# Optimization experiments

Measured on AMD Instinct MI355X. Metric: run time of the kernel, lower is better.

Reference implementation:

```python
import jax, jax.numpy as jnp
import numpy as np
from jax import lax

FILTERS = 8

def _conv(x, k):
    # x: (B,H,W,Cin), k: (KH,KW,Cin,Cout), SAME padding, stride 1
    return lax.conv_general_dilated(x, k, (1, 1), 'SAME',
                                    dimension_numbers=('NHWC', 'HWIO', 'NHWC'))

def _hard_sigmoid(x):
    # keras hard_sigmoid: clip(0.2*x + 0.5, 0, 1)
    return jnp.clip(0.2 * x + 0.5, 0.0, 1.0)


def setup_inputs() -> dict:
    key = jax.random.key(0)
    ks = jax.random.split(key, 4)
    B, T, H, W, C = 32, 16, 64, 64, 3
    x = jax.random.normal(ks[0], (B, T, H, W, C), dtype=jnp.float32)
    W_x = jax.random.normal(ks[1], (3, 3, C, 4 * FILTERS), dtype=jnp.float32) * 0.1
    W_h = jax.random.normal(ks[2], (3, 3, FILTERS, 4 * FILTERS), dtype=jnp.float32) * 0.1
    b = jnp.zeros((4 * FILTERS,), dtype=jnp.float32)
    W_out = jax.random.normal(ks[3], (H * W * FILTERS, 4), dtype=jnp.float32) * 0.02
    b_out = jnp.zeros((4,), dtype=jnp.float32)
    return {"x": x, "W_x": W_x, "W_h": W_h, "b": b, "W_out": W_out, "b_out": b_out}


def reference(x, W_x, W_h, b, W_out, b_out):
    B, T, H, W, C = x.shape
    F = FILTERS

    def step(carry, xt):
        h, c = carry
        z = _conv(xt, W_x) + _conv(h, W_h) + b  # (B,H,W,4F)
        zi, zf, zc, zo = jnp.split(z, 4, axis=-1)  # keras gate order: i, f, c, o
        i = _hard_sigmoid(zi)
        f = _hard_sigmoid(zf)
        c = f * c + i * jnp.tanh(zc)
        o = _hard_sigmoid(zo)
        h = o * jnp.tanh(c)
        return (h, c), None

    h0 = jnp.zeros((B, H, W, F), dtype=x.dtype)
    c0 = jnp.zeros((B, H, W, F), dtype=x.dtype)
    xs = jnp.moveaxis(x, 1, 0)  # (T,B,H,W,C)
    (h_final, _), _ = lax.scan(step, (h0, c0), xs)

    flat = h_final.reshape(B, -1)  # (B, H*W*F)
    logits = flat @ W_out + b_out
    return jax.nn.softmax(logits, axis=-1)
```

## Files before the change

### kernel.cpp

```cpp
#include <hip/hip_runtime.h>
#include <math.h>

#define NB 32
#define NT 16

typedef _Float16 f16;
typedef _Float16 half2f __attribute__((ext_vector_type(2)));
typedef _Float16 half4f __attribute__((ext_vector_type(4)));
typedef _Float16 half8f __attribute__((ext_vector_type(8)));
typedef float    floatx2 __attribute__((ext_vector_type(2)));
typedef float    floatx4 __attribute__((ext_vector_type(4)));

#define XPAD_OFF  0u
#define HPAD0_OFF 18382848u
#define HPAD1_OFF 20680704u
#define CBUF_OFF  22978560u
#define WBQ_OFF   27172864u
#define PART_OFF  27181056u
#define WS_NEED   27197440u

#define BAND0   0
#define BAND1   10880
#define CLDS_OFF 21760
#define REDF_OFF 38144
#define SMEM4    38272

__device__ __forceinline__ float hard_sigmoid(float v) {
    return fminf(fmaxf(fmaf(0.2f, v, 0.5f), 0.0f), 1.0f);
}
__device__ __forceinline__ float fast_tanh(float v) {
    float e = __builtin_amdgcn_exp2f(v * 2.8853900817779268f);
    return 1.0f - 2.0f * __builtin_amdgcn_rcpf(e + 1.0f);
}

__device__ __forceinline__ float wb_entry(int i, const float* Wx,
                                          const float* Wh, const float* bias) {
    int e = i & 7, l = (i >> 3) & 63, n = (i >> 9) & 1, j = i >> 10;
    int h = l >> 4;
    int rr = l & 15;
    int g = (rr & 3) * 8 + 2 * (rr >> 2) + n;
    float wv = 0.f;
    if (j == 0) {
        wv = Wh[(h * 8 + e) * 32 + g];
    } else if (j == 1) {
        wv = Wh[((4 + h) * 8 + e) * 32 + g];
    } else if (j == 2 && h == 0) {
        wv = Wh[(64 + e) * 32 + g];
    } else if (j == 3 && h == 3) {
        wv = (e == 3) ? bias[g] : 0.f;
    } else {
        int ty, txp;
        if (j == 2) { ty = (h == 3) ? 1 : 0; txp = (h == 2) ? 2 : 0; }
        else        { ty = (h == 0) ? 1 : 2; txp = (h == 1) ? 0 : 2; }
        int txq = txp + (e >> 2), c = e & 3;
        if (txq < 3 && c < 3)
            wv = Wx[((ty * 3 + txq) * 3 + c) * 32 + g];
    }
    return wv;
}

#define LDX(base, off) ({                                                  \
    half4f lo_ = *(const half4f*)((base) + (off));                         \
    half4f hi_ = *(const half4f*)((base) + (off) + 8);                     \
    __builtin_shufflevector(lo_, hi_, 0, 1, 2, 3, 4, 5, 6, 7); })

#define GATE_BODY(A0, A1, A2, A3, COLD0, COLD1, CC0, CC1, HH0, HH1)        \
    {                                                                      \
        floatx4 acc0 = {0.f, 0.f, 0.f, 0.f};                               \
        floatx4 acc1 = {0.f, 0.f, 0.f, 0.f};                               \
        acc0 = __builtin_amdgcn_mfma_f32_16x16x32_f16(B00, A0, acc0,0,0,0);\
        acc1 = __builtin_amdgcn_mfma_f32_16x16x32_f16(B01, A0, acc1,0,0,0);\
        acc0 = __builtin_amdgcn_mfma_f32_16x16x32_f16(B10, A1, acc0,0,0,0);\
        acc1 = __builtin_amdgcn_mfma_f32_16x16x32_f16(B11, A1, acc1,0,0,0);\
        acc0 = __builtin_amdgcn_mfma_f32_16x16x32_f16(B20, A2, acc0,0,0,0);\
        acc1 = __builtin_amdgcn_mfma_f32_16x16x32_f16(B21, A2, acc1,0,0,0);\
        acc0 = __builtin_amdgcn_mfma_f32_16x16x32_f16(B30, A3, acc0,0,0,0);\
        acc1 = __builtin_amdgcn_mfma_f32_16x16x32_f16(B31, A3, acc1,0,0,0);\
        float ig0 = hard_sigmoid(acc0[0]), fg0 = hard_sigmoid(acc0[1]);    \
        float cg0 = fast_tanh(acc0[2]),    og0 = hard_sigmoid(acc0[3]);    \
        CC0 = fmaf(fg0, COLD0, ig0 * cg0);                                 \
        HH0 = og0 * fast_tanh(CC0);                                        \
        float ig1 = hard_sigmoid(acc1[0]), fg1 = hard_sigmoid(acc1[1]);    \
        float cg1 = fast_tanh(acc1[2]),    og1 = hard_sigmoid(acc1[3]);    \
        CC1 = fmaf(fg1, COLD1, ig1 * cg1);                                 \
        HH1 = og1 * fast_tanh(CC1);                                        \
    }

__global__ __launch_bounds__(256) void init_all(
    const float* __restrict__ x,
    const float* __restrict__ Wx, const float* __restrict__ Wh,
    const float* __restrict__ bias,
    f16* __restrict__ xpad, f16* __restrict__ h0, f16* __restrict__ h1,
    f16* __restrict__ WB)
{
    int i = blockIdx.x * 256 + threadIdx.x;
    if (i < 200704) {
        int bt = i / 392, p = i - bt * 392;
        int rr, cc;
        if (p < 136) { rr = (p < 68) ? 0 : 65; cc = p - ((p < 68) ? 0 : 68); }
        else { int q = p - 136; rr = 1 + (q >> 2); int m = q & 3;
               cc = (m == 0) ? 0 : 64 + m; }
        half4f v = {0, 0, 0, (f16)1.0f};
        *(half4f*)(xpad + ((size_t)(bt * 66 + rr) * 68 + cc) * 4) = v;
    } else if (i < 225792) {
        int k = i - 200704;
        int buf = k / 12544; k -= buf * 12544;
        int b = k / 392, p = k - b * 392;
        int rr, cc;
        if (p < 136) { rr = (p < 68) ? 0 : 65; cc = p - ((p < 68) ? 0 : 68); }
        else { int q = p - 136; rr = 1 + (q >> 2); int m = q & 3;
               cc = (m == 0) ? 0 : 64 + m; }
        f16* hp = buf ? h1 : h0;
        half8f zz = {0, 0, 0, 0, 0, 0, 0, 0};
        *(half8f*)(hp + ((size_t)(b * 66 + rr) * 68 + cc) * 8) = zz;
    } else if (i < 229888) {
        int k = i - 225792;
        WB[k] = (f16)wb_entry(k, Wx, Wh, bias);
    } else if (i < 754176) {
        int j = i - 229888;
        int b = j >> 14;
        int rem = j & 16383;
        int s = rem >> 12, px = rem & 4095;
        const float* xp = x + ((size_t)(b * 16 + s) * 4096 + px) * 3;
        half4f v = {(f16)xp[0], (f16)xp[1], (f16)xp[2], (f16)1.0f};
        int gr = px >> 6, gc = px & 63;
        *(half4f*)(xpad + ((size_t)((b * 16 + s) * 66 + gr + 1) * 68 + gc + 1) * 4) = v;
    }
}

__global__ __launch_bounds__(512, 4) void convlstm_fused4(
    const float* __restrict__ x,
    f16* __restrict__ xpad,
    const f16* __restrict__ WB,
    const f16* __restrict__ h_in,
    f16* __restrict__ h_out,
    float* __restrict__ c_buf,
    const float* __restrict__ Wout,
    float* __restrict__ partial,
    int t, int first, int do_head)
{
    __shared__ __attribute__((aligned(16))) char smem[SMEM4];

    const int bid0 = blockIdx.x;
    const int bid  = ((bid0 & 7) << 6) | (bid0 >> 3);
    const int bi  = bid >> 4;
    const int r0  = (bid & 15) << 2;
    const int tid = threadIdx.x;
    const int w    = __builtin_amdgcn_readfirstlane(tid >> 6);
    const int lane = tid & 63;
    const int p16  = lane & 15;
    const int g4   = lane >> 4;
    const int f0   = g4 << 1;

    const int c0s = t + 4 + (tid >> 8);
    const int c1s = c0s + 2;
    const bool c0v = (c0s < NT), c1v = (c1s < NT);
    const int c0p = tid & 255, c1p = c0p;
    const int c0r = r0 + (c0p >> 6), c0c = c0p & 63;
    float c0x0 = 0.f, c0x1 = 0.f, c0x2 = 0.f;
    float c1x0 = 0.f, c1x1 = 0.f, c1x2 = 0.f;
    if (c0v) {
        const float* p = x + ((size_t)(bi * NT + c0s) * 4096 + c0r * 64 + c0c) * 3;
        c0x0 = p[0]; c0x1 = p[1]; c0x2 = p[2];
    }
    if (c1v) {
        const float* p = x + ((size_t)(bi * NT + c1s) * 4096 + c0r * 64 + c0c) * 3;
        c1x0 = p[0]; c1x1 = p[1]; c1x2 = p[2];
    }

    const half8f* WBv = (const half8f*)WB;
    half8f B00 = WBv[0*64+lane], B01 = WBv[1*64+lane];
    half8f B10 = WBv[2*64+lane], B11 = WBv[3*64+lane];
    half8f B20 = WBv[4*64+lane], B21 = WBv[5*64+lane];
    half8f B30 = WBv[6*64+lane], B31 = WBv[7*64+lane];

    const int ty0 = (g4 >= 3) ? 1 : 0, tx0 = g4 - 3 * ty0;
    const int ty1 = 1 + ((g4 >= 2) ? 1 : 0), tx1 = (g4 + 4) - 3 * ty1;
    const int ty2 = (g4 == 3) ? 1 : 0, tx2 = (g4 == 2) ? 2 : 0;
    const int ty3 = (g4 == 0) ? 1 : 2, tx3 = (g4 == 1) ? 0 : 2;

    const half8f z8 = {0, 0, 0, 0, 0, 0, 0, 0};

    if (tid < 40) {
        int buf = tid / 20;
        int rr  = (tid % 20) >> 1;
        int cc  = (tid & 1) ? 65 : 0;
        *(half8f*)(smem + (buf ? BAND1 : BAND0) + (rr * 68 + cc) * 16) = z8;
    }

    {
        #pragma unroll
        for (int k = 0; k < 5; ++k) {
            const int tau = w * 5 + k;
            const int rowl = tau >> 2, ct = tau & 3;
            const int row = r0 - 3 + rowl;
            const bool vA = ((unsigned)row < 64u);
            const int colA = ct * 16 + p16;
            float cc0 = 0.f, cc1 = 0.f, hh0 = 0.f, hh1 = 0.f;
            if (vA) {
                floatx2 cold = {0.f, 0.f};
                if (!first)
                    cold = *(const floatx2*)(c_buf +
                               ((size_t)(bi * 4096 + row * 64 + colA)) * 8 + f0);
                const char* hpA = (const char*)(h_in + ((size_t)(bi * 66 + row)) * 68 * 8);
                const char* xpA = (const char*)(xpad +
                    ((size_t)((bi * 16 + t) * 66 + row)) * 68 * 4);
                half8f a0 = first ? z8 : *(const half8f*)(hpA + (ty0 * 68 + colA + tx0) * 16);
                half8f a1 = first ? z8 : *(const half8f*)(hpA + (ty1 * 68 + colA + tx1) * 16);
                half8f a2;
                if (g4 == 0) a2 = first ? z8 : *(const half8f*)(hpA + (2 * 68 + colA + 2) * 16);
                else         a2 = LDX(xpA, (ty2 * 68 + colA + tx2) * 8);
                half8f a3 = LDX(xpA, (ty3 * 68 + colA + tx3) * 8);
                GATE_BODY(a0, a1, a2, a3, cold[0], cold[1], cc0, cc1, hh0, hh1);
            }
            half2f hw = {(f16)hh0, (f16)hh1};
            *(half2f*)(smem + BAND0 + (rowl * 68 + 1 + colA) * 16 + f0 * 2) = hw;
            if (rowl >= 1 && rowl <= 8) {
                floatx2 cw = {cc0, cc1};
                *(floatx2*)(smem + CLDS_OFF + (((rowl - 1) * 64 + colA) * 8 + f0) * 4) = cw;
            }
        }
    }
    __syncthreads();

    {
        #pragma unroll
        for (int k = 0; k < 4; ++k) {
            const int tau = w * 4 + k;
            const int rowl = tau >> 2, ct = tau & 3;
            const int row = r0 - 2 + rowl;
            const bool vA = ((unsigned)row < 64u);
            const int colA = ct * 16 + p16;
            const int cidx = rowl;
            float cc0 = 0.f, cc1 = 0.f, hh0 = 0.f, hh1 = 0.f;
            if (vA) {
                floatx2 cold = *(const floatx2*)(smem + CLDS_OFF +
                                   ((cidx * 64 + colA) * 8 + f0) * 4);
                const char* xpA = (const char*)(xpad +
                    ((size_t)((bi * 16 + t + 1) * 66 + row)) * 68 * 4);
                half8f a0 = *(const half8f*)(smem + BAND0 + ((rowl + ty0) * 68 + colA + tx0) * 16);
                half8f a1 = *(const half8f*)(smem + BAND0 + ((rowl + ty1) * 68 + colA + tx1) * 16);
                half8f a2;
                if (g4 == 0) a2 = *(const half8f*)(smem + BAND0 + ((rowl + 2) * 68 + colA + 2) * 16);
                else         a2 = LDX(xpA, (ty2 * 68 + colA + tx2) * 8);
                half8f a3 = LDX(xpA, (ty3 * 68 + colA + tx3) * 8);
                GATE_BODY(a0, a1, a2, a3, cold[0], cold[1], cc0, cc1, hh0, hh1);
            }
            half2f hw = {(f16)hh0, (f16)hh1};
            *(half2f*)(smem + BAND1 + ((rowl + 1) * 68 + 1 + colA) * 16 + f0 * 2) = hw;
            floatx2 cw = {cc0, cc1};
            *(floatx2*)(smem + CLDS_OFF + ((cidx * 64 + colA) * 8 + f0) * 4) = cw;
        }
    }
    __syncthreads();

    {
        #pragma unroll
        for (int k = 0; k < 3; ++k) {
            const int tau = w * 3 + k;
            const int rowl = tau >> 2, ct = tau & 3;
            const int row = r0 - 1 + rowl;
            const bool vA = ((unsigned)row < 64u);
            const int colA = ct * 16 + p16;
            const int cidx = rowl + 1;
            float cc0 = 0.f, cc1 = 0.f, hh0 = 0.f, hh1 = 0.f;
            if (vA) {
                floatx2 cold = *(const floatx2*)(smem + CLDS_OFF +
                                   ((cidx * 64 + colA) * 8 + f0) * 4);
                const char* xpA = (const char*)(xpad +
                    ((size_t)((bi * 16 + t + 2) * 66 + row)) * 68 * 4);
                half8f a0 = *(const half8f*)(smem + BAND1 + ((rowl + 1 + ty0) * 68 + colA + tx0) * 16);
                half8f a1 = *(const half8f*)(smem + BAND1 + ((rowl + 1 + ty1) * 68 + colA + tx1) * 16);
                half8f a2;
                if (g4 == 0) a2 = *(const half8f*)(smem + BAND1 + ((rowl + 3) * 68 + colA + 2) * 16);
                else         a2 = LDX(xpA, (ty2 * 68 + colA + tx2) * 8);
                half8f a3 = LDX(xpA, (ty3 * 68 + colA + tx3) * 8);
                GATE_BODY(a0, a1, a2, a3, cold[0], cold[1], cc0, cc1, hh0, hh1);
            }
            half2f hw = {(f16)hh0, (f16)hh1};
            *(half2f*)(smem + BAND0 + ((rowl + 2) * 68 + 1 + colA) * 16 + f0 * 2) = hw;
            floatx2 cw = {cc0, cc1};
            *(floatx2*)(smem + CLDS_OFF + ((cidx * 64 + colA) * 8 + f0) * 4) = cw;
        }
    }
    __syncthreads();

    {
        float ha0 = 0.f, ha1 = 0.f, ha2 = 0.f, ha3 = 0.f;
        #pragma unroll
        for (int k = 0; k < 2; ++k) {
            const int tau = w * 2 + k;
            const int rowl = tau >> 2, ct = tau & 3;
            const int row = r0 + rowl;
            const int colA = ct * 16 + p16;
            const int cidx = rowl + 2;
            floatx2 cold = *(const floatx2*)(smem + CLDS_OFF +
                               ((cidx * 64 + colA) * 8 + f0) * 4);
            const char* xpA = (const char*)(xpad +
                ((size_t)((bi * 16 + t + 3) * 66 + row)) * 68 * 4);
            half8f a0 = *(const half8f*)(smem + BAND0 + ((rowl + 2 + ty0) * 68 + colA + tx0) * 16);
            half8f a1 = *(const half8f*)(smem + BAND0 + ((rowl + 2 + ty1) * 68 + colA + tx1) * 16);
            half8f a2;
            if (g4 == 0) a2 = *(const half8f*)(smem + BAND0 + ((rowl + 4) * 68 + colA + 2) * 16);
            else         a2 = LDX(xpA, (ty2 * 68 + colA + tx2) * 8);
            half8f a3 = LDX(xpA, (ty3 * 68 + colA + tx3) * 8);
            float cc0, cc1, hh0, hh1;
            GATE_BODY(a0, a1, a2, a3, cold[0], cold[1], cc0, cc1, hh0, hh1);

            if (!do_head) {
                const size_t gp = (size_t)(bi * 4096 + row * 64 + colA);
                floatx2 cw = {cc0, cc1};
                *(floatx2*)(c_buf + gp * 8 + f0) = cw;
                const size_t hb = ((size_t)(bi * 66 + row + 1) * 68 + 1 + colA) * 8 + f0;
                half2f hw = {(f16)hh0, (f16)hh1};
                *(half2f*)(h_out + hb) = hw;
            } else {
                int pix = row * 64 + colA;
                floatx4 wa  = *(const floatx4*)(Wout + (size_t)(pix * 8 + f0) * 4);
                floatx4 wb2 = *(const floatx4*)(Wout + (size_t)(pix * 8 + f0 + 1) * 4);
                ha0 = fmaf(hh0, wa[0], fmaf(hh1, wb2[0], ha0));
                ha1 = fmaf(hh0, wa[1], fmaf(hh1, wb2[1], ha1));
                ha2 = fmaf(hh0, wa[2], fmaf(hh1, wb2[2], ha2));
                ha3 = fmaf(hh0, wa[3], fmaf(hh1, wb2[3], ha3));
            }
        }

        if (do_head) {
            #pragma unroll
            for (int off = 32; off >= 1; off >>= 1) {
                ha0 += __shfl_down(ha0, off, 64);
                ha1 += __shfl_down(ha1, off, 64);
                ha2 += __shfl_down(ha2, off, 64);
                ha3 += __shfl_down(ha3, off, 64);
            }
            if (lane == 0) {
                floatx4 v = {ha0, ha1, ha2, ha3};
                *(floatx4*)(smem + REDF_OFF + w * 16) = v;
            }
            __syncthreads();
            if (tid == 0) {
                floatx4 s = {0.f, 0.f, 0.f, 0.f};
                #pragma unroll
                for (int k = 0; k < 8; ++k)
                    s += *(const floatx4*)(smem + REDF_OFF + k * 16);
                *(floatx4*)(partial + (size_t)bid * 4) = s;
            }
        }
    }

    if (c0v) {
        half4f v = {(f16)c0x0, (f16)c0x1, (f16)c0x2, (f16)1.0f};
        *(half4f*)(xpad + ((size_t)((bi * 16 + c0s) * 66 + c0r + 1) * 68 + c0c + 1) * 4) = v;
    }
    if (c1v) {
        half4f v = {(f16)c1x0, (f16)c1x1, (f16)c1x2, (f16)1.0f};
        *(half4f*)(xpad + ((size_t)((bi * 16 + c1s) * 66 + c0r + 1) * 68 + c0c + 1) * 4) = v;
    }
}

__global__ __launch_bounds__(64) void head_finish(
    const float* __restrict__ partial,
    const float* __restrict__ bout,
    float* __restrict__ out)
{
    int b = threadIdx.x;
    if (b >= NB) return;
    float l0 = bout[0], l1 = bout[1], l2 = bout[2], l3 = bout[3];
    for (int s = 0; s < 16; ++s) {
        floatx4 p = *(const floatx4*)(partial + (size_t)(b * 16 + s) * 4);
        l0 += p[0]; l1 += p[1]; l2 += p[2]; l3 += p[3];
    }
    float m = fmaxf(fmaxf(l0, l1), fmaxf(l2, l3));
    float e0 = expf(l0 - m), e1 = expf(l1 - m);
    float e2 = expf(l2 - m), e3 = expf(l3 - m);
    float inv = 1.0f / (e0 + e1 + e2 + e3);
    out[b * 4 + 0] = e0 * inv;
    out[b * 4 + 1] = e1 * inv;
    out[b * 4 + 2] = e2 * inv;
    out[b * 4 + 3] = e3 * inv;
}

__global__ __launch_bounds__(256) void prepack_fb(
    const float* __restrict__ Wx, const float* __restrict__ Wh,
    const float* __restrict__ bias, f16* __restrict__ WB)
{
    int i = blockIdx.x * 256 + threadIdx.x;
    if (i < 4096) WB[i] = (f16)wb_entry(i, Wx, Wh, bias);
}

#define FB_XOFF 4352
#define FB_SMEM 6528

#define LDAS(off) ({                                                       \
    half4f lo_ = *(const half4f*)(smem + (off));                           \
    half4f hi_ = *(const half4f*)(smem + (off) + 8);                       \
    __builtin_shufflevector(lo_, hi_, 0, 1, 2, 3, 4, 5, 6, 7); })

__global__ __launch_bounds__(256, 4) void convlstm_step_fb(
    const float* __restrict__ x, const f16* __restrict__ WB,
    const f16* __restrict__ h_in, f16* __restrict__ h_out,
    float* __restrict__ c_buf, int t, int first)
{
    __shared__ __attribute__((aligned(16))) char smem[FB_SMEM];

    const int bid = blockIdx.x;
    const int bi  = bid >> 5;
    const int r0  = (bid & 31) << 1;
    const int tid = threadIdx.x;
    const int w    = tid >> 6;
    const int lane = tid & 63;
    const int p16  = lane & 15;
    const int g4   = lane >> 4;
    const int pr   = w >> 1;
    const int wcol = (w & 1) << 5;

    const float* xt = x + (((size_t)bi * NT + t) * 4096) * 3;

    for (int i = tid; i < 272; i += 256) {
        int lr = i / 68, lc = i - lr * 68;
        int gr = r0 - 1 + lr, gc = lc - 1;
        bool ok = ((unsigned)gr < 64u) && ((unsigned)gc < 64u);
        half4f xv = {0, 0, 0, (f16)1.0f};
        half8f hv = {0, 0, 0, 0, 0, 0, 0, 0};
        if (ok) {
            const float* xp = xt + (gr * 64 + gc) * 3;
            xv[0] = (f16)xp[0]; xv[1] = (f16)xp[1]; xv[2] = (f16)xp[2];
            if (!first)
                hv = *(const half8f*)(h_in + ((size_t)(bi * 4096 + gr * 64 + gc)) * 8);
        }
        *(half8f*)(smem + i * 16) = hv;
        *(half4f*)(smem + FB_XOFF + i * 8) = xv;
    }

    const half8f* WBv = (const half8f*)WB;
    half8f B00 = WBv[0*64+lane], B01 = WBv[1*64+lane];
    half8f B10 = WBv[2*64+lane], B11 = WBv[3*64+lane];
    half8f B20 = WBv[4*64+lane], B21 = WBv[5*64+lane];
    half8f B30 = WBv[6*64+lane], B31 = WBv[7*64+lane];

    const int f0 = g4 << 1;
    const size_t gp0 = (size_t)(bi * 4096 + (r0 + pr) * 64 + wcol + p16);
    const size_t gp1 = gp0 + 16;
    floatx2 cold0 = {0.f, 0.f}, cold1 = {0.f, 0.f};
    if (!first) {
        cold0 = *(const floatx2*)(c_buf + gp0 * 8 + f0);
        cold1 = *(const floatx2*)(c_buf + gp1 * 8 + f0);
    }

    __syncthreads();

    const int ty0 = (g4 >= 3) ? 1 : 0, tx0 = g4 - 3 * ty0;
    const int ty1 = 1 + ((g4 >= 2) ? 1 : 0), tx1 = (g4 + 4) - 3 * ty1;
    const int ty2 = (g4 == 3) ? 1 : 0, tx2 = (g4 == 2) ? 2 : 0;
    const int ty3 = (g4 == 0) ? 1 : 2, tx3 = (g4 == 1) ? 0 : 2;
    const int inc2 = (g4 == 0) ? 256 : 128;
    int o0 = ((pr + ty0) * 68 + wcol + p16 + tx0) * 16;
    int o1 = ((pr + ty1) * 68 + wcol + p16 + tx1) * 16;
    int o2 = (g4 == 0) ? ((pr + 2) * 68 + wcol + p16 + 2) * 16
                       : FB_XOFF + ((pr + ty2) * 68 + wcol + p16 + tx2) * 8;
    int o3 = FB_XOFF + ((pr + ty3) * 68 + wcol + p16 + tx3) * 8;

    #pragma unroll
    for (int tt = 0; tt < 2; ++tt) {
        half8f a0 = LDAS(o0), a1 = LDAS(o1), a2 = LDAS(o2), a3 = LDAS(o3);
        floatx2 cold = tt ? cold1 : cold0;
        float cc0, cc1, hh0, hh1;
        GATE_BODY(a0, a1, a2, a3, cold[0], cold[1], cc0, cc1, hh0, hh1);
        const size_t gp = tt ? gp1 : gp0;
        floatx2 cw = {cc0, cc1};
        *(floatx2*)(c_buf + gp * 8 + f0) = cw;
        half2f hw = {(f16)hh0, (f16)hh1};
        *(half2f*)(h_out + gp * 8 + f0) = hw;
        o0 += 256; o1 += 256; o2 += inc2; o3 += 128;
    }
}

__global__ __launch_bounds__(256) void head_partial_fb(
    const f16* __restrict__ h, const float* __restrict__ Wout,
    float* __restrict__ partial)
{
    const int b = blockIdx.x >> 4;
    const int chunk = blockIdx.x & 15;
    const int tid = threadIdx.x;
    const f16* hb = h + (size_t)b * 32768 + chunk * 2048;
    const float* wb = Wout + (size_t)(chunk * 2048) * 4;

    float acc[4] = {0.f, 0.f, 0.f, 0.f};
    #pragma unroll
    for (int it = 0; it < 8; ++it) {
        int i = it * 256 + tid;
        float hv = (float)hb[i];
        float4 wv = *(const float4*)(wb + (size_t)i * 4);
        acc[0] = fmaf(hv, wv.x, acc[0]);
        acc[1] = fmaf(hv, wv.y, acc[1]);
        acc[2] = fmaf(hv, wv.z, acc[2]);
        acc[3] = fmaf(hv, wv.w, acc[3]);
    }
    #pragma unroll
    for (int j = 0; j < 4; ++j)
        #pragma unroll
        for (int off = 32; off >= 1; off >>= 1)
            acc[j] += __shfl_down(acc[j], off, 64);

    __shared__ float red2[4][4];
    int lane = tid & 63, wv2 = tid >> 6;
    if (lane == 0) {
        #pragma unroll
        for (int j = 0; j < 4; ++j) red2[wv2][j] = acc[j];
    }
    __syncthreads();
    if (tid == 0) {
        #pragma unroll
        for (int j = 0; j < 4; ++j)
            partial[(size_t)blockIdx.x * 4 + j] =
                red2[0][j] + red2[1][j] + red2[2][j] + red2[3][j];
    }
}

__global__ __launch_bounds__(64) void head_finish_fb(
    const float* __restrict__ partial, const float* __restrict__ bout,
    float* __restrict__ out)
{
    int b = threadIdx.x;
    if (b >= NB) return;
    float logit[4] = {bout[0], bout[1], bout[2], bout[3]};
    #pragma unroll
    for (int k = 0; k < 16; ++k) {
        const float* p = partial + (size_t)(b * 16 + k) * 4;
        logit[0] += p[0]; logit[1] += p[1]; logit[2] += p[2]; logit[3] += p[3];
    }
    float m = fmaxf(fmaxf(logit[0], logit[1]), fmaxf(logit[2], logit[3]));
    float e[4], s = 0.f;
    #pragma unroll
    for (int j = 0; j < 4; ++j) { e[j] = expf(logit[j] - m); s += e[j]; }
    float inv = 1.0f / s;
    #pragma unroll
    for (int j = 0; j < 4; ++j) out[b * 4 + j] = e[j] * inv;
}

extern "C" void kernel_launch(void* const* d_in, const int* in_sizes, int n_in,
                              void* d_out, int out_size, void* d_ws, size_t ws_size,
                              hipStream_t stream) {
    const float* x    = (const float*)d_in[0];
    const float* Wx   = (const float*)d_in[1];
    const float* Wh   = (const float*)d_in[2];
    const float* b    = (const float*)d_in[3];
    const float* Wout = (const float*)d_in[4];
    const float* bout = (const float*)d_in[5];
    float* out = (float*)d_out;
    char* ws = (char*)d_ws;

    if (ws_size >= WS_NEED) {
        f16*   xpad  = (f16*)(ws + XPAD_OFF);
        f16*   h0    = (f16*)(ws + HPAD0_OFF);
        f16*   h1    = (f16*)(ws + HPAD1_OFF);
        float* cb    = (float*)(ws + CBUF_OFF);
        f16*   WBq   = (f16*)(ws + WBQ_OFF);
        float* part  = (float*)(ws + PART_OFF);

        init_all<<<2946, 256, 0, stream>>>(x, Wx, Wh, b, xpad, h0, h1, WBq);

        for (int k = 0; k < 4; ++k) {
            const f16* hin  = (k & 1) ? h0 : h1;
            f16*       hout = (k & 1) ? h1 : h0;
            convlstm_fused4<<<512, 512, 0, stream>>>(
                x, xpad, WBq, hin, hout, cb, Wout, part,
                4 * k, (k == 0) ? 1 : 0, (k == 3) ? 1 : 0);
        }
        head_finish<<<1, 64, 0, stream>>>(part, bout, out);
    } else {
        f16*   hA      = (f16*)ws;
        f16*   hB      = (f16*)(ws + (1u << 21));
        float* cb      = (float*)(ws + (1u << 22));
        f16*   WBq     = (f16*)(ws + (1u << 23));
        float* partial = (float*)(ws + (1u << 23) + 8192);

        prepack_fb<<<16, 256, 0, stream>>>(Wx, Wh, b, WBq);
        for (int t = 0; t < NT; ++t) {
            const f16* hin = (t & 1) ? hA : hB;
            f16*       hout = (t & 1) ? hB : hA;
            convlstm_step_fb<<<1024, 256, 0, stream>>>(x, WBq, hin, hout, cb,
                                                       t, (t == 0) ? 1 : 0);
        }
        head_partial_fb<<<512, 256, 0, stream>>>(hB, Wout, partial);
        head_finish_fb<<<1, 64, 0, stream>>>(partial, bout, out);
    }
}
```

Measured before the change: 77.34 us.

## Double rows per block in fused 4-step ConvLSTM kernel to cut halo recompute

Each block now covers 8 output rows instead of 4, using 1024 threads and 256 blocks. This lowers the fraction of redundant halo-row recomputation across the four fused timesteps and halves the number of head partials. The cost is larger LDS bands, heavier block-wide barriers, and fewer blocks, which may hurt occupancy and load balance.

Measured after the change: 65.77 us. 1.18x faster.

```diff
diff --git a/kernel.cpp b/kernel.cpp
--- a/kernel.cpp
+++ b/kernel.cpp
@@ -19,11 +19,11 @@
 #define PART_OFF  27181056u
 #define WS_NEED   27197440u
 
-#define BAND0   0
-#define BAND1   10880
-#define CLDS_OFF 21760
-#define REDF_OFF 38144
-#define SMEM4    38272
+#define BANDA   0
+#define BANDB   15232
+#define CLDS4   30464
+#define REDF4   55040
+#define SMEM5   55296
 
 __device__ __forceinline__ float hard_sigmoid(float v) {
     return fminf(fmaxf(fmaf(0.2f, v, 0.5f), 0.0f), 1.0f);
@@ -128,7 +128,7 @@
     }
 }
 
-__global__ __launch_bounds__(512, 4) void convlstm_fused4(
+__global__ __launch_bounds__(1024, 4) void convlstm_fused4w(
     const float* __restrict__ x,
     f16* __restrict__ xpad,
     const f16* __restrict__ WB,
@@ -139,12 +139,12 @@
     float* __restrict__ partial,
     int t, int first, int do_head)
 {
-    __shared__ __attribute__((aligned(16))) char smem[SMEM4];
+    __shared__ __attribute__((aligned(16))) char smem[SMEM5];
 
     const int bid0 = blockIdx.x;
-    const int bid  = ((bid0 & 7) << 6) | (bid0 >> 3);
-    const int bi  = bid >> 4;
-    const int r0  = (bid & 15) << 2;
+    const int bid  = ((bid0 & 7) << 5) | (bid0 >> 3);
+    const int bi  = bid >> 3;
+    const int r0  = (bid & 7) << 3;
     const int tid = threadIdx.x;
     const int w    = __builtin_amdgcn_readfirstlane(tid >> 6);
     const int lane = tid & 63;
@@ -152,20 +152,16 @@
     const int g4   = lane >> 4;
     const int f0   = g4 << 1;
 
-    const int c0s = t + 4 + (tid >> 8);
-    const int c1s = c0s + 2;
-    const bool c0v = (c0s < NT), c1v = (c1s < NT);
-    const int c0p = tid & 255, c1p = c0p;
-    const int c0r = r0 + (c0p >> 6), c0c = c0p & 63;
-    float c0x0 = 0.f, c0x1 = 0.f, c0x2 = 0.f;
-    float c1x0 = 0.f, c1x1 = 0.f, c1x2 = 0.f;
-    if (c0v) {
-        const float* p = x + ((size_t)(bi * NT + c0s) * 4096 + c0r * 64 + c0c) * 3;
-        c0x0 = p[0]; c0x1 = p[1]; c0x2 = p[2];
-    }
-    if (c1v) {
-        const float* p = x + ((size_t)(bi * NT + c1s) * 4096 + c0r * 64 + c0c) * 3;
-        c1x0 = p[0]; c1x1 = p[1]; c1x2 = p[2];
+    const int csl = t + 4 + (tid >> 8);
+    const bool cv = (csl < NT);
+    const int cpb = (tid & 255) << 1;
+    const int cgr = r0 + (cpb >> 6), cgc = cpb & 63;
+    float cxa0 = 0.f, cxa1 = 0.f, cxa2 = 0.f;
+    float cxb0 = 0.f, cxb1 = 0.f, cxb2 = 0.f;
+    if (cv) {
+        const float* p = x + ((size_t)(bi * NT + csl) * 4096 + cgr * 64 + cgc) * 3;
+        cxa0 = p[0]; cxa1 = p[1]; cxa2 = p[2];
+        cxb0 = p[3]; cxb1 = p[4]; cxb2 = p[5];
     }
 
     const half8f* WBv = (const half8f*)WB;
@@ -181,19 +177,19 @@
 
     const half8f z8 = {0, 0, 0, 0, 0, 0, 0, 0};
 
-    if (tid < 40) {
-        int buf = tid / 20;
-        int rr  = (tid % 20) >> 1;
+    if (tid < 56) {
+        int buf = tid / 28;
+        int r2  = (tid % 28) >> 1;
         int cc  = (tid & 1) ? 65 : 0;
-        *(half8f*)(smem + (buf ? BAND1 : BAND0) + (rr * 68 + cc) * 16) = z8;
-    }
-
-    {
-        #pragma unroll
-        for (int k = 0; k < 5; ++k) {
-            const int tau = w * 5 + k;
-            const int rowl = tau >> 2, ct = tau & 3;
-            const int row = r0 - 3 + rowl;
+        *(half8f*)(smem + (buf ? BANDB : BANDA) + (r2 * 68 + cc) * 16) = z8;
+    }
+
+    #pragma unroll
+    for (int k = 0; k < 4; ++k) {
+        const int tau = k * 16 + w;
+        if (tau < 56) {
+            const int bl = tau >> 2, ct = tau & 3;
+            const int row = r0 - 3 + bl;
             const bool vA = ((unsigned)row < 64u);
             const int colA = ct * 16 + p16;
             float cc0 = 0.f, cc1 = 0.f, hh0 = 0.f, hh1 = 0.f;
@@ -214,73 +210,69 @@
                 GATE_BODY(a0, a1, a2, a3, cold[0], cold[1], cc0, cc1, hh0, hh1);
             }
             half2f hw = {(f16)hh0, (f16)hh1};
-            *(half2f*)(smem + BAND0 + (rowl * 68 + 1 + colA) * 16 + f0 * 2) = hw;
-            if (rowl >= 1 && rowl <= 8) {
+            *(half2f*)(smem + BANDA + (bl * 68 + 1 + colA) * 16 + f0 * 2) = hw;
+            if (bl >= 1 && bl <= 12) {
                 floatx2 cw = {cc0, cc1};
-                *(floatx2*)(smem + CLDS_OFF + (((rowl - 1) * 64 + colA) * 8 + f0) * 4) = cw;
+                *(floatx2*)(smem + CLDS4 + (((bl - 1) * 64 + colA) * 8 + f0) * 4) = cw;
             }
         }
     }
     __syncthreads();
 
-    {
-        #pragma unroll
-        for (int k = 0; k < 4; ++k) {
-            const int tau = w * 4 + k;
-            const int rowl = tau >> 2, ct = tau & 3;
-            const int row = r0 - 2 + rowl;
+    #pragma unroll
+    for (int k = 0; k < 3; ++k) {
+        const int tau = k * 16 + w;
+        const int bl = 1 + (tau >> 2), ct = tau & 3;
+        const int row = r0 - 3 + bl;
+        const bool vA = ((unsigned)row < 64u);
+        const int colA = ct * 16 + p16;
+        float cc0 = 0.f, cc1 = 0.f, hh0 = 0.f, hh1 = 0.f;
+        if (vA) {
+            floatx2 cold = *(const floatx2*)(smem + CLDS4 +
+                               (((bl - 1) * 64 + colA) * 8 + f0) * 4);
+            const char* xpA = (const char*)(xpad +
+                ((size_t)((bi * 16 + t + 1) * 66 + row)) * 68 * 4);
+            half8f a0 = *(const half8f*)(smem + BANDA + ((bl - 1 + ty0) * 68 + colA + tx0) * 16);
+            half8f a1 = *(const half8f*)(smem + BANDA + ((bl - 1 + ty1) * 68 + colA + tx1) * 16);
+            half8f a2;
+            if (g4 == 0) a2 = *(const half8f*)(smem + BANDA + ((bl + 1) * 68 + colA + 2) * 16);
+            else         a2 = LDX(xpA, (ty2 * 68 + colA + tx2) * 8);
+            half8f a3 = LDX(xpA, (ty3 * 68 + colA + tx3) * 8);
+            GATE_BODY(a0, a1, a2, a3, cold[0], cold[1], cc0, cc1, hh0, hh1);
+        }
+        half2f hw = {(f16)hh0, (f16)hh1};
+        *(half2f*)(smem + BANDB + (bl * 68 + 1 + colA) * 16 + f0 * 2) = hw;
+        floatx2 cw = {cc0, cc1};
+        *(floatx2*)(smem + CLDS4 + (((bl - 1) * 64 + colA) * 8 + f0) * 4) = cw;
+    }
+    __syncthreads();
+
+    #pragma unroll
+    for (int k = 0; k < 3; ++k) {
+        const int tau = k * 16 + w;
+        if (tau < 40) {
+            const int bl = 2 + (tau >> 2), ct = tau & 3;
+            const int row = r0 - 3 + bl;
             const bool vA = ((unsigned)row < 64u);
             const int colA = ct * 16 + p16;
-            const int cidx = rowl;
             float cc0 = 0.f, cc1 = 0.f, hh0 = 0.f, hh1 = 0.f;
             if (vA) {
-                floatx2 cold = *(const floatx2*)(smem + CLDS_OFF +
-                                   ((cidx * 64 + colA) * 8 + f0) * 4);
+                floatx2 cold = *(const floatx2*)(smem + CLDS4 +
+                                   (((bl - 1) * 64 + colA) * 8 + f0) * 4);
                 const char* xpA = (const char*)(xpad +
-                    ((size_t)((bi * 16 + t + 1) * 66 + row)) * 68 * 4);
-                half8f a0 = *(const half8f*)(smem + BAND0 + ((rowl + ty0) * 68 + colA + tx0) * 16);
-                half8f a1 = *(const half8f*)(smem + BAND0 + ((rowl + ty1) * 68 + colA + tx1) * 16);
+                    ((size_t)((bi * 16 + t + 2) * 66 + row)) * 68 * 4);
+                half8f a0 = *(const half8f*)(smem + BANDB + ((bl - 1 + ty0) * 68 + colA + tx0) * 16);
+                half8f a1 = *(const half8f*)(smem + BANDB + ((bl - 1 + ty1) * 68 + colA + tx1) * 16);
                 half8f a2;
-                if (g4 == 0) a2 = *(const half8f*)(smem + BAND0 + ((rowl + 2) * 68 + colA + 2) * 16);
+                if (g4 == 0) a2 = *(const half8f*)(smem + BANDB + ((bl + 1) * 68 + colA + 2) * 16);
                 else         a2 = LDX(xpA, (ty2 * 68 + colA + tx2) * 8);
                 half8f a3 = LDX(xpA, (ty3 * 68 + colA + tx3) * 8);
                 GATE_BODY(a0, a1, a2, a3, cold[0], cold[1], cc0, cc1, hh0, hh1);
             }
             half2f hw = {(f16)hh0, (f16)hh1};
-            *(half2f*)(smem + BAND1 + ((rowl + 1) * 68 + 1 + colA) * 16 + f0 * 2) = hw;
+            *(half2f*)(smem + BANDA + (bl * 68 + 1 + colA) * 16 + f0 * 2) = hw;
             floatx2 cw = {cc0, cc1};
-            *(floatx2*)(smem + CLDS_OFF + ((cidx * 64 + colA) * 8 + f0) * 4) = cw;
-        }
-    }
-    __syncthreads();
-
-    {
-        #pragma unroll
-        for (int k = 0; k < 3; ++k) {
-            const int tau = w * 3 + k;
-            const int rowl = tau >> 2, ct = tau & 3;
-            const int row = r0 - 1 + rowl;
-            const bool vA = ((unsigned)row < 64u);
-            const int colA = ct * 16 + p16;
-            const int cidx = rowl + 1;
-            float cc0 = 0.f, cc1 = 0.f, hh0 = 0.f, hh1 = 0.f;
-            if (vA) {
-                floatx2 cold = *(const floatx2*)(smem + CLDS_OFF +
-                                   ((cidx * 64 + colA) * 8 + f0) * 4);
-                const char* xpA = (const char*)(xpad +
-                    ((size_t)((bi * 16 + t + 2) * 66 + row)) * 68 * 4);
-                half8f a0 = *(const half8f*)(smem + BAND1 + ((rowl + 1 + ty0) * 68 + colA + tx0) * 16);
-                half8f a1 = *(const half8f*)(smem + BAND1 + ((rowl + 1 + ty1) * 68 + colA + tx1) * 16);
-                half8f a2;
-                if (g4 == 0) a2 = *(const half8f*)(smem + BAND1 + ((rowl + 3) * 68 + colA + 2) * 16);
-                else         a2 = LDX(xpA, (ty2 * 68 + colA + tx2) * 8);
-                half8f a3 = LDX(xpA, (ty3 * 68 + colA + tx3) * 8);
-                GATE_BODY(a0, a1, a2, a3, cold[0], cold[1], cc0, cc1, hh0, hh1);
-            }
-            half2f hw = {(f16)hh0, (f16)hh1};
-            *(half2f*)(smem + BAND0 + ((rowl + 2) * 68 + 1 + colA) * 16 + f0 * 2) = hw;
-            floatx2 cw = {cc0, cc1};
-            *(floatx2*)(smem + CLDS_OFF + ((cidx * 64 + colA) * 8 + f0) * 4) = cw;
+            *(floatx2*)(smem + CLDS4 + (((bl - 1) * 64 + colA) * 8 + f0) * 4) = cw;
         }
     }
     __syncthreads();
@@ -289,19 +281,18 @@
         float ha0 = 0.f, ha1 = 0.f, ha2 = 0.f, ha3 = 0.f;
         #pragma unroll
         for (int k = 0; k < 2; ++k) {
-            const int tau = w * 2 + k;
-            const int rowl = tau >> 2, ct = tau & 3;
-            const int row = r0 + rowl;
+            const int tau = k * 16 + w;
+            const int bl = 3 + (tau >> 2), ct = tau & 3;
+            const int row = r0 - 3 + bl;
             const int colA = ct * 16 + p16;
-            const int cidx = rowl + 2;
-            floatx2 cold = *(const floatx2*)(smem + CLDS_OFF +
-                               ((cidx * 64 + colA) * 8 + f0) * 4);
+            floatx2 cold = *(const floatx2*)(smem + CLDS4 +
+                               (((bl - 1) * 64 + colA) * 8 + f0) * 4);
             const char* xpA = (const char*)(xpad +
                 ((size_t)((bi * 16 + t + 3) * 66 + row)) * 68 * 4);
-            half8f a0 = *(const half8f*)(smem + BAND0 + ((rowl + 2 + ty0) * 68 + colA + tx0) * 16);
-            half8f a1 = *(const half8f*)(smem + BAND0 + ((rowl + 2 + ty1) * 68 + colA + tx1) * 16);
+            half8f a0 = *(const half8f*)(smem + BANDA + ((bl - 1 + ty0) * 68 + colA + tx0) * 16);
+            half8f a1 = *(const half8f*)(smem + BANDA + ((bl - 1 + ty1) * 68 + colA + tx1) * 16);
             half8f a2;
-            if (g4 == 0) a2 = *(const half8f*)(smem + BAND0 + ((rowl + 4) * 68 + colA + 2) * 16);
+            if (g4 == 0) a2 = *(const half8f*)(smem + BANDA + ((bl + 1) * 68 + colA + 2) * 16);
             else         a2 = LDX(xpA, (ty2 * 68 + colA + tx2) * 8);
             half8f a3 = LDX(xpA, (ty3 * 68 + colA + tx3) * 8);
             float cc0, cc1, hh0, hh1;
@@ -335,26 +326,25 @@
             }
             if (lane == 0) {
                 floatx4 v = {ha0, ha1, ha2, ha3};
-                *(floatx4*)(smem + REDF_OFF + w * 16) = v;
+                *(floatx4*)(smem + REDF4 + w * 16) = v;
             }
             __syncthreads();
             if (tid == 0) {
                 floatx4 s = {0.f, 0.f, 0.f, 0.f};
                 #pragma unroll
-                for (int k = 0; k < 8; ++k)
-                    s += *(const floatx4*)(smem + REDF_OFF + k * 16);
+                for (int k = 0; k < 16; ++k)
+                    s += *(const floatx4*)(smem + REDF4 + k * 16);
                 *(floatx4*)(partial + (size_t)bid * 4) = s;
             }
         }
     }
 
-    if (c0v) {
-        half4f v = {(f16)c0x0, (f16)c0x1, (f16)c0x2, (f16)1.0f};
-        *(half4f*)(xpad + ((size_t)((bi * 16 + c0s) * 66 + c0r + 1) * 68 + c0c + 1) * 4) = v;
-    }
-    if (c1v) {
-        half4f v = {(f16)c1x0, (f16)c1x1, (f16)c1x2, (f16)1.0f};
-        *(half4f*)(xpad + ((size_t)((bi * 16 + c1s) * 66 + c0r + 1) * 68 + c0c + 1) * 4) = v;
+    if (cv) {
+        f16* dst = xpad + ((size_t)((bi * 16 + csl) * 66 + cgr + 1) * 68 + cgc + 1) * 4;
+        half4f va = {(f16)cxa0, (f16)cxa1, (f16)cxa2, (f16)1.0f};
+        half4f vb = {(f16)cxb0, (f16)cxb1, (f16)cxb2, (f16)1.0f};
+        *(half4f*)(dst)     = va;
+        *(half4f*)(dst + 4) = vb;
     }
 }
 
@@ -366,8 +356,8 @@
     int b = threadIdx.x;
     if (b >= NB) return;
     float l0 = bout[0], l1 = bout[1], l2 = bout[2], l3 = bout[3];
-    for (int s = 0; s < 16; ++s) {
-        floatx4 p = *(const floatx4*)(partial + (size_t)(b * 16 + s) * 4);
+    for (int s = 0; s < 8; ++s) {
+        floatx4 p = *(const floatx4*)(partial + (size_t)(b * 8 + s) * 4);
         l0 += p[0]; l1 += p[1]; l2 += p[2]; l3 += p[3];
     }
     float m = fmaxf(fmaxf(l0, l1), fmaxf(l2, l3));
@@ -563,7 +553,7 @@
         for (int k = 0; k < 4; ++k) {
             const f16* hin  = (k & 1) ? h0 : h1;
             f16*       hout = (k & 1) ? h1 : h0;
-            convlstm_fused4<<<512, 512, 0, stream>>>(
+            convlstm_fused4w<<<256, 1024, 0, stream>>>(
                 x, xpad, WBq, hin, hout, cb, Wout, part,
                 4 * k, (k == 0) ? 1 : 0, (k == 3) ? 1 : 0);
         }
```
